# Performance work log

Hardware: AMD Instinct MI355X
Metric: run time of the kernel (lower is better)

Reference implementation:

```python
import jax, jax.numpy as jnp
import numpy as np

B, T, A, I, H = 256, 128, 4, 128, 256


def setup_inputs() -> dict:
    key = jax.random.key(0)
    ks = jax.random.split(key, 6)
    x = jax.random.normal(ks[0], (B, T, A, I), jnp.float32)
    is_init = jax.random.randint(ks[1], (B, T, 1), 0, 2).astype(bool)
    s = 1.0 / np.sqrt(H)  # torch GRUCell init range
    W_ih = jax.random.uniform(ks[2], (3 * H, I), jnp.float32, -s, s)
    W_hh = jax.random.uniform(ks[3], (3 * H, H), jnp.float32, -s, s)
    b_ih = jax.random.uniform(ks[4], (3 * H,), jnp.float32, -s, s)
    b_hh = jax.random.uniform(ks[5], (3 * H,), jnp.float32, -s, s)
    return dict(x=x, is_init=is_init, W_ih=W_ih, W_hh=W_hh, b_ih=b_ih, b_hh=b_hh)


def _gru_forward(x, is_init, W_ih, W_hh, b_ih, b_hh):
    Bb, Tt, Aa, Ii = x.shape
    Hh = W_hh.shape[1]
    # Precompute input projections for all steps: [B,T,A,3H]
    gi = jnp.einsum('btai,ki->btak', x, W_ih) + b_ih
    # is_init [B,T,1] -> per-agent reset mask [B,T,A,1]
    init = jnp.broadcast_to(is_init[:, :, None, :], (Bb, Tt, Aa, 1))
    h0 = jnp.zeros((Bb, Aa, Hh), x.dtype)

    def step(h, inp):
        gi_t, init_t = inp  # [B,A,3H], [B,A,1]
        h = jnp.where(init_t, 0.0, h)  # per-step reset before the cell
        gh = jnp.einsum('bah,kh->bak', h, W_hh) + b_hh
        i_r, i_z, i_n = jnp.split(gi_t, 3, axis=-1)
        h_r, h_z, h_n = jnp.split(gh, 3, axis=-1)
        r = jax.nn.sigmoid(i_r + h_r)
        z = jax.nn.sigmoid(i_z + h_z)
        n = jnp.tanh(i_n + r * h_n)
        h_new = (1.0 - z) * n + z * h
        return h_new, h_new

    _, hs = jax.lax.scan(step, h0, (jnp.moveaxis(gi, 1, 0), jnp.moveaxis(init, 1, 0)))
    return jnp.moveaxis(hs, 0, 1)  # [B,T,A,H]


def reference(x, is_init, W_ih, W_hh, b_ih, b_hh):
    output = _gru_forward(x, is_init, W_ih, W_hh, b_ih, b_hh)
    h_n = output[:, -1]  # [B,A,H]
    return (output, h_n)
```

## Files before the change

kernel.cpp:

```cpp
#include <hip/hip_runtime.h>
#include <cstdint>
#include <cstddef>

#define BB 256
#define TT 128
#define AA 4
#define II 128
#define HH 256
#define K3 768

typedef __attribute__((ext_vector_type(8))) short short8;
typedef __attribute__((ext_vector_type(4))) float f32x4;
typedef __attribute__((ext_vector_type(4))) unsigned short ushort4_t;

#define LGKM_BARRIER() asm volatile("s_waitcnt lgkmcnt(0)\n\ts_barrier" ::: "memory")

static __device__ __forceinline__ unsigned short f2bf(float f) {
  unsigned int b = __float_as_uint(f);
  return (unsigned short)((b + 0x7FFFu + ((b >> 16) & 1u)) >> 16);
}
static __device__ __forceinline__ float bf2f(unsigned short u) {
  return __uint_as_float(((unsigned int)u) << 16);
}

__global__ void wconv_kernel(const float* __restrict__ wih,
                             const float* __restrict__ whh,
                             unsigned short* __restrict__ o) {
  int i = blockIdx.x * 512 + threadIdx.x;
  float v = (i < K3 * II) ? wih[i] : whh[i - K3 * II];
  o[i] = f2bf(v);
}

__global__ __launch_bounds__(512, 2) void gi_kernel(
    const float* __restrict__ x,
    const float* __restrict__ bih_g,
    const float* __restrict__ bhh_g,
    const unsigned short* __restrict__ wb,
    unsigned short* __restrict__ gi) {
  __shared__ alignas(16) unsigned short xs[64][144];
  __shared__ alignas(16) unsigned short gst[16][792];
  __shared__ float bihs[K3];

  const int tid = threadIdx.x;
  const int l = tid & 63, w = tid >> 6;
  const int c = l & 15, g = l >> 4;
  const size_t m0 = (size_t)blockIdx.x * 64;

  for (int i = tid; i < K3; i += 512)
    bihs[i] = bih_g[i] + (i < 2 * HH ? bhh_g[i] : 0.f);
  for (int i = tid; i < 64 * 128; i += 512) {
    int row = i >> 7, col = i & 127;
    xs[row][col] = f2bf(x[m0 * 128 + i]);
  }
  short8 wf[6][4];
#pragma unroll
  for (int kt = 0; kt < 6; ++kt) {
    int row = 96 * w + kt * 16 + c;
#pragma unroll
    for (int kk = 0; kk < 4; ++kk)
      wf[kt][kk] = *(const short8*)&wb[(size_t)row * II + kk * 32 + g * 8];
  }
  LGKM_BARRIER();

  for (int chunk = 0; chunk < 4; ++chunk) {
    short8 bx[4];
#pragma unroll
    for (int kk = 0; kk < 4; ++kk)
      bx[kk] = *(const short8*)&xs[chunk * 16 + c][kk * 32 + g * 8];
    f32x4 acc[6];
#pragma unroll
    for (int kt = 0; kt < 6; ++kt) acc[kt] = (f32x4){0.f, 0.f, 0.f, 0.f};
#pragma unroll
    for (int kt = 0; kt < 6; ++kt)
#pragma unroll
      for (int kk = 0; kk < 4; ++kk)
        acc[kt] = __builtin_amdgcn_mfma_f32_16x16x32_bf16(wf[kt][kk], bx[kk], acc[kt], 0, 0, 0);
#pragma unroll
    for (int kt = 0; kt < 6; ++kt) {
      int gate0 = 96 * w + kt * 16 + g * 4;
      ushort4_t p;
#pragma unroll
      for (int r = 0; r < 4; ++r) p[r] = f2bf(acc[kt][r] + bihs[gate0 + r]);
      *(ushort4_t*)&gst[c][gate0] = p;
    }
    LGKM_BARRIER();
    for (int i = tid; i < 16 * 96; i += 512) {
      int row = i / 96, seg = i - row * 96;
      *(short8*)(gi + (m0 + chunk * 16 + row) * K3 + seg * 8) =
          *(const short8*)&gst[row][seg * 8];
    }
    LGKM_BARRIER();
  }
}

__global__ __launch_bounds__(512, 2) void rnn_kernel(
    const void* __restrict__ init_raw,
    const float* __restrict__ bhh_g,
    const unsigned short* __restrict__ wsb,
    const unsigned short* __restrict__ gi,
    float* __restrict__ out) {
  extern __shared__ char smem[];
  unsigned short* wlN = (unsigned short*)smem;
  unsigned short* hsb = (unsigned short*)(smem + 131072);
  float* scr = (float*)(smem + 135168);
  unsigned char* msk = (unsigned char*)(smem + 147968);
  int* detf = (int*)(smem + 148096);

  const int tid = threadIdx.x;
  const int b = blockIdx.x;
  const unsigned short* whh_b = wsb + K3 * II;

  if (tid < 3) detf[tid] = 0;
  for (int i = tid; i < 2048; i += 512) hsb[i] = 0;
  for (int e = tid; e < 8192; e += 512) {
    int w2 = e >> 10, n = (e >> 9) & 1, kk = (e >> 6) & 7, l2 = e & 63;
    int row = 512 + 32 * w2 + 16 * n + (l2 & 15);
    int col = kk * 32 + (l2 >> 4) * 8;
    *(short8*)(wlN + (size_t)e * 8) = *(const short8*)&whh_b[(size_t)row * HH + col];
  }

  {
    const unsigned int* wq = (const unsigned int*)init_raw;
    int notf = 0, gt1 = 0, oddnz = 0;
    for (int i = tid; i < (BB * TT / 4); i += 512) {
      unsigned int v = wq[i];
      notf |= (v != 0u && v != 0x3F800000u);
      gt1 |= (v > 1u);
      if (i & 1) oddnz |= (v != 0u);
    }
    if (notf) atomicOr(&detf[0], 1);
    if (gt1) atomicOr(&detf[1], 1);
    if (oddnz) atomicOr(&detf[2], 1);
  }
  __syncthreads();
  if (tid < TT) {
    int layout = (!detf[0]) ? 1 : (detf[1] ? 0 : (detf[2] ? 1 : 2));
    int e = b * TT + tid;
    unsigned int v;
    if (layout == 0)      v = ((const unsigned char*)init_raw)[e];
    else if (layout == 1) v = ((const unsigned int*)init_raw)[e];
    else                  v = ((const unsigned int*)init_raw)[2 * e];
    msk[tid] = v ? 1 : 0;
  }

  const int l = tid & 63, w = tid >> 6;
  const int c = l & 15, g = l >> 4;
  const bool act = (c < AA);

  short8 wreg[4][8];
#pragma unroll
  for (int q = 0; q < 4; ++q) {
    int row = (q >> 1) * 256 + 32 * w + (q & 1) * 16 + c;
#pragma unroll
    for (int kk = 0; kk < 8; ++kk)
      wreg[q][kk] = *(const short8*)&whh_b[(size_t)row * HH + kk * 32 + g * 8];
  }

  const int a = g;
  const int u2 = 2 * c;
  const int j0 = 32 * w + u2;
  const float2 bn2 = *(const float2*)&bhh_g[2 * HH + j0];

  __syncthreads();

  const unsigned short* gp = gi + ((size_t)(b * TT) * AA + a) * K3 + j0;
  float* op = out + ((size_t)(b * TT) * AA + a) * HH + j0;
  const unsigned short* hrd = hsb + ((c & 3) * 4 + g) * 8;
  unsigned short* hwp = hsb + w * 128 + a * 32 + u2;
  float* swp = scr + w * 400 + c * 100 + g * 4;
  const float* srp = scr + w * 400 + a * 100 + u2;
  const unsigned short* wlp = wlN + w * 8192 + l * 8;

  float h0 = 0.f, h1 = 0.f;
  unsigned int gcA[3], gcB[3];
  int mA, mB;
  const f32x4 Z4 = {0.f, 0.f, 0.f, 0.f};

#define GI_LOAD(GC)                               \
  do {                                            \
    GC[0] = *(const unsigned int*)(gp);           \
    GC[1] = *(const unsigned int*)(gp + 256);     \
    GC[2] = *(const unsigned int*)(gp + 512);     \
    gp += AA * K3;                                \
  } while (0)

#define L2E 1.44269504088896f

#define STEP(P, GC, MK)                                                           \
  do {                                                                            \
    float sR0, sR1, sZ0, sZ1, sN0, sN1;                                           \
    if ((MK) != 0) {                                                              \
      h0 = 0.f; h1 = 0.f;                                                         \
      sR0 = sR1 = sZ0 = sZ1 = sN0 = sN1 = 0.f;                                    \
    } else {                                                                      \
      short8 bhf[8];                                                              \
      _Pragma("unroll") for (int kk = 0; kk < 8; ++kk)                            \
          bhf[kk] = *(const short8*)(hrd + (P) * 1024 + kk * 128);                \
      f32x4 aR0 = __builtin_amdgcn_mfma_f32_16x16x32_bf16(wreg[0][0], bhf[0], Z4, 0, 0, 0); \
      f32x4 aR1 = __builtin_amdgcn_mfma_f32_16x16x32_bf16(wreg[1][0], bhf[0], Z4, 0, 0, 0); \
      f32x4 aZ0 = __builtin_amdgcn_mfma_f32_16x16x32_bf16(wreg[2][0], bhf[0], Z4, 0, 0, 0); \
      f32x4 aZ1 = __builtin_amdgcn_mfma_f32_16x16x32_bf16(wreg[3][0], bhf[0], Z4, 0, 0, 0); \
      f32x4 aN0 = __builtin_amdgcn_mfma_f32_16x16x32_bf16(                        \
          *(const short8*)(wlp), bhf[0], Z4, 0, 0, 0);                            \
      f32x4 aN1 = __builtin_amdgcn_mfma_f32_16x16x32_bf16(                        \
          *(const short8*)(wlp + 4096), bhf[0], Z4, 0, 0, 0);                     \
      _Pragma("unroll") for (int kk = 1; kk < 8; ++kk) {                          \
        aR0 = __builtin_amdgcn_mfma_f32_16x16x32_bf16(wreg[0][kk], bhf[kk], aR0, 0, 0, 0); \
        aR1 = __builtin_amdgcn_mfma_f32_16x16x32_bf16(wreg[1][kk], bhf[kk], aR1, 0, 0, 0); \
        aZ0 = __builtin_amdgcn_mfma_f32_16x16x32_bf16(wreg[2][kk], bhf[kk], aZ0, 0, 0, 0); \
        aZ1 = __builtin_amdgcn_mfma_f32_16x16x32_bf16(wreg[3][kk], bhf[kk], aZ1, 0, 0, 0); \
        aN0 = __builtin_amdgcn_mfma_f32_16x16x32_bf16(                            \
            *(const short8*)(wlp + kk * 512), bhf[kk], aN0, 0, 0, 0);             \
        aN1 = __builtin_amdgcn_mfma_f32_16x16x32_bf16(                            \
            *(const short8*)(wlp + 4096 + kk * 512), bhf[kk], aN1, 0, 0, 0);      \
      }                                                                           \
      if (act) {                                                                  \
        *(f32x4*)(swp + 0)  = aR0;                                                \
        *(f32x4*)(swp + 16) = aR1;                                                \
        *(f32x4*)(swp + 32) = aZ0;                                                \
        *(f32x4*)(swp + 48) = aZ1;                                                \
        *(f32x4*)(swp + 64) = aN0;                                                \
        *(f32x4*)(swp + 80) = aN1;                                                \
      }                                                                           \
      float2 vR = *(const float2*)(srp);                                          \
      float2 vZ = *(const float2*)(srp + 32);                                     \
      float2 vN = *(const float2*)(srp + 64);                                     \
      sR0 = vR.x; sR1 = vR.y; sZ0 = vZ.x; sZ1 = vZ.y; sN0 = vN.x; sN1 = vN.y;     \
    }                                                                             \
    const float gr0 = bf2f((unsigned short)(GC[0]));                              \
    const float gr1 = bf2f((unsigned short)(GC[0] >> 16));                        \
    const float gz0 = bf2f((unsigned short)(GC[1]));                              \
    const float gz1 = bf2f((unsigned short)(GC[1] >> 16));                        \
    const float gn0 = bf2f((unsigned short)(GC[2]));                              \
    const float gn1 = bf2f((unsigned short)(GC[2] >> 16));                        \
    const float rs0 = __builtin_amdgcn_rcpf(1.f + __builtin_amdgcn_exp2f(-(gr0 + sR0) * L2E)); \
    const float rs1 = __builtin_amdgcn_rcpf(1.f + __builtin_amdgcn_exp2f(-(gr1 + sR1) * L2E)); \
    const float zs0 = __builtin_amdgcn_rcpf(1.f + __builtin_amdgcn_exp2f(-(gz0 + sZ0) * L2E)); \
    const float zs1 = __builtin_amdgcn_rcpf(1.f + __builtin_amdgcn_exp2f(-(gz1 + sZ1) * L2E)); \
    const float pre0 = gn0 + rs0 * (sN0 + bn2.x);                                 \
    const float pre1 = gn1 + rs1 * (sN1 + bn2.y);                                 \
    const float nn0 = 1.f - 2.f * __builtin_amdgcn_rcpf(1.f + __builtin_amdgcn_exp2f(pre0 * (2.f * L2E))); \
    const float nn1 = 1.f - 2.f * __builtin_amdgcn_rcpf(1.f + __builtin_amdgcn_exp2f(pre1 * (2.f * L2E))); \
    h0 = fmaf(zs0, h0 - nn0, nn0);                                                \
    h1 = fmaf(zs1, h1 - nn1, nn1);                                                \
    unsigned int hw = (unsigned int)f2bf(h0) | ((unsigned int)f2bf(h1) << 16);    \
    *(unsigned int*)(hwp + (1 - (P)) * 1024) = hw;                                \
    float2 o2; o2.x = h0; o2.y = h1;                                              \
    *(float2*)op = o2;                                                            \
    op += AA * HH;                                                                \
    LGKM_BARRIER();                                                               \
  } while (0)

  GI_LOAD(gcA);
  mA = msk[0];
  for (int t = 0; t < TT - 2; t += 2) {
    GI_LOAD(gcB);
    mB = msk[t + 1];
    STEP(0, gcA, mA);
    GI_LOAD(gcA);
    mA = msk[t + 2];
    STEP(1, gcB, mB);
  }
  {
    GI_LOAD(gcB);
    mB = msk[TT - 1];
    STEP(0, gcA, mA);
    STEP(1, gcB, mB);
  }

  {
    float* hp = out + (size_t)BB * TT * AA * HH + ((size_t)b * AA + a) * HH + j0;
    float2 o2; o2.x = h0; o2.y = h1;
    *(float2*)hp = o2;
  }
#undef GI_LOAD
#undef STEP
}

template <int WSW>
__global__ __launch_bounds__(512, 2) void gru_kernel(
    const float* __restrict__ x,
    const void* __restrict__ init_raw,
    const float* __restrict__ wih_f,
    const float* __restrict__ whh_f,
    const float* __restrict__ bih_g,
    const float* __restrict__ bhh_g,
    const unsigned short* __restrict__ wb,
    float* __restrict__ out) {
  __shared__ alignas(16) unsigned short xs[AA][II + 8];
  __shared__ alignas(16) unsigned short hsb[AA][HH + 8];
  __shared__ float hs32[AA][HH];
  __shared__ float gi_s[K3][5];
  __shared__ float gh_s[K3][5];
  __shared__ float bihs[K3];
  __shared__ float bhhs[K3];
  __shared__ unsigned char msk[TT];
  __shared__ int detf[3];

  const int tid = threadIdx.x;
  const int b = blockIdx.x;

  if (tid < 3) detf[tid] = 0;
  for (int i = tid; i < K3; i += 512) { bihs[i] = bih_g[i]; bhhs[i] = bhh_g[i]; }
  for (int i = tid; i < AA * HH; i += 512) {
    hs32[i >> 8][i & 255] = 0.f;
    hsb[i >> 8][i & 255] = 0;
  }
  __syncthreads();
  {
    const unsigned int* wq = (const unsigned int*)init_raw;
    int notf = 0, gt1 = 0, oddnz = 0;
    for (int i = tid; i < (BB * TT / 4); i += 512) {
      unsigned int v = wq[i];
      notf |= (v != 0u && v != 0x3F800000u);
      gt1 |= (v > 1u);
      if (i & 1) oddnz |= (v != 0u);
    }
    if (notf) atomicOr(&detf[0], 1);
    if (gt1) atomicOr(&detf[1], 1);
    if (oddnz) atomicOr(&detf[2], 1);
  }
  __syncthreads();
  if (tid < TT) {
    int layout = (!detf[0]) ? 1 : (detf[1] ? 0 : (detf[2] ? 1 : 2));
    int e = b * TT + tid;
    unsigned int v;
    if (layout == 0)      v = ((const unsigned char*)init_raw)[e];
    else if (layout == 1) v = ((const unsigned int*)init_raw)[e];
    else                  v = ((const unsigned int*)init_raw)[2 * e];
    msk[tid] = v ? 1 : 0;
  }
  __syncthreads();

  const int l = tid & 63;
  const int w = tid >> 6;
  const int c = l & 15;
  const int g = l >> 4;
  const bool act = (c < AA);
  const int xa = tid >> 7, xi = tid & 127;
  const float* xrow = x + (size_t)b * TT * AA * II;
  const unsigned short* wihb = wb;
  const unsigned short* whhb = wb + K3 * II;

  for (int t = 0; t < TT; ++t) {
    xs[xa][xi] = f2bf(xrow[(size_t)t * (AA * II) + tid]);
    if (msk[t]) {
      for (int i = tid; i < AA * HH; i += 512) {
        hs32[i >> 8][i & 255] = 0.f;
        hsb[i >> 8][i & 255] = 0;
      }
    }
    __syncthreads();

    short8 bx[4], bh[8];
    if (act) {
#pragma unroll
      for (int kk = 0; kk < 4; ++kk) bx[kk] = *(const short8*)&xs[c][kk * 32 + g * 8];
#pragma unroll
      for (int kk = 0; kk < 8; ++kk) bh[kk] = *(const short8*)&hsb[c][kk * 32 + g * 8];
    } else {
#pragma unroll
      for (int kk = 0; kk < 4; ++kk) bx[kk] = (short8)0;
#pragma unroll
      for (int kk = 0; kk < 8; ++kk) bh[kk] = (short8)0;
    }

#pragma unroll
    for (int kt = 0; kt < 6; ++kt) {
      const int ar = w * 96 + kt * 16 + c;
      f32x4 acc = {0.f, 0.f, 0.f, 0.f};
#pragma unroll
      for (int kk = 0; kk < 4; ++kk) {
        short8 aw;
        if (WSW) {
          aw = *(const short8*)&wihb[(size_t)ar * II + kk * 32 + g * 8];
        } else {
          const float* p = &wih_f[(size_t)ar * II + kk * 32 + g * 8];
#pragma unroll
          for (int e = 0; e < 8; ++e) aw[e] = (short)f2bf(p[e]);
        }
        acc = __builtin_amdgcn_mfma_f32_16x16x32_bf16(aw, bx[kk], acc, 0, 0, 0);
      }
      if (act) {
        const int dr = w * 96 + kt * 16 + g * 4;
#pragma unroll
        for (int r = 0; r < 4; ++r) gi_s[dr + r][c] = acc[r];
      }
    }

#pragma unroll
    for (int kt = 0; kt < 6; ++kt) {
      const int ar = w * 96 + kt * 16 + c;
      f32x4 acc = {0.f, 0.f, 0.f, 0.f};
#pragma unroll
      for (int kk = 0; kk < 8; ++kk) {
        short8 aw;
        if (WSW) {
          aw = *(const short8*)&whhb[(size_t)ar * HH + kk * 32 + g * 8];
        } else {
          const float* p = &whh_f[(size_t)ar * HH + kk * 32 + g * 8];
#pragma unroll
          for (int e = 0; e < 8; ++e) aw[e] = (short)f2bf(p[e]);
        }
        acc = __builtin_amdgcn_mfma_f32_16x16x32_bf16(aw, bh[kk], acc, 0, 0, 0);
      }
      if (act) {
        const int dr = w * 96 + kt * 16 + g * 4;
#pragma unroll
        for (int r = 0; r < 4; ++r) gh_s[dr + r][c] = acc[r];
      }
    }
    __syncthreads();

#pragma unroll
    for (int it = 0; it < 2; ++it) {
      const int idx = it * 512 + tid;
      const int a = idx >> 8, j = idx & 255;
      const float ir = gi_s[j][a] + bihs[j];
      const float iz = gi_s[HH + j][a] + bihs[HH + j];
      const float inn = gi_s[2 * HH + j][a] + bihs[2 * HH + j];
      const float hr = gh_s[j][a] + bhhs[j];
      const float hz = gh_s[HH + j][a] + bhhs[HH + j];
      const float hn = gh_s[2 * HH + j][a] + bhhs[2 * HH + j];
      const float r = 1.f / (1.f + __expf(-(ir + hr)));
      const float z = 1.f / (1.f + __expf(-(iz + hz)));
      const float pre = inn + r * hn;
      const float ea = __expf(-2.f * fabsf(pre));
      float n = (1.f - ea) / (1.f + ea);
      n = (pre < 0.f) ? -n : n;
      const float hold = hs32[a][j];
      const float hnew = (1.f - z) * n + z * hold;
      hs32[a][j] = hnew;
      hsb[a][j] = f2bf(hnew);
      out[(((size_t)b * TT + t) * AA + a) * HH + j] = hnew;
      if (t == TT - 1)
        out[(size_t)BB * TT * AA * HH + ((size_t)b * AA + a) * HH + j] = hnew;
    }
    __syncthreads();
  }
}

extern "C" void kernel_launch(void* const* d_in, const int* in_sizes, int n_in,
                              void* d_out, int out_size, void* d_ws, size_t ws_size,
                              hipStream_t stream) {
  (void)in_sizes; (void)n_in; (void)out_size;
  const float* x = (const float*)d_in[0];
  const void* is_init = d_in[1];
  const float* wih = (const float*)d_in[2];
  const float* whh = (const float*)d_in[3];
  const float* bih = (const float*)d_in[4];
  const float* bhh = (const float*)d_in[5];
  float* out = (float*)d_out;

  const size_t W_ELS = (size_t)(K3 * II + K3 * HH);
  const size_t W_BYTES = W_ELS * 2;
  const size_t GI_BYTES = (size_t)BB * TT * AA * K3 * 2;
  const int SMEM = 148112;

  if (ws_size >= W_BYTES + GI_BYTES) {
    hipError_t e = hipFuncSetAttribute(
        (const void*)rnn_kernel, hipFuncAttributeMaxDynamicSharedMemorySize, SMEM);
    if (e == hipSuccess) {
      unsigned short* wb = (unsigned short*)d_ws;
      unsigned short* gi = wb + W_ELS;
      wconv_kernel<<<(int)(W_ELS / 512), 512, 0, stream>>>(wih, whh, wb);
      gi_kernel<<<2048, 512, 0, stream>>>(x, bih, bhh, wb, gi);
      rnn_kernel<<<BB, 512, SMEM, stream>>>(is_init, bhh, wb, gi, out);
      return;
    }
  }
  if (ws_size >= W_BYTES) {
    unsigned short* wb = (unsigned short*)d_ws;
    wconv_kernel<<<(int)(W_ELS / 512), 512, 0, stream>>>(wih, whh, wb);
    gru_kernel<1><<<BB, 512, 0, stream>>>(x, is_init, wih, whh, bih, bhh, wb, out);
  } else {
    gru_kernel<0><<<BB, 512, 0, stream>>>(x, is_init, wih, whh, bih, bhh, nullptr, out);
  }
}
```

Baseline: 243.8 us.

## Split each sequence into independent segments at reset points and run them concurrently

Every reset in the mask sets the hidden state to zero, so the sequence is cut at the first reset after positions 32, 64 and 96 into up to four independent segments. These segments fill the 12 MFMA columns that were previously padding (only 4 of 16 were used). The recurrence then runs for only the longest segment length instead of all 128 steps. It also removes the scratch round-trip through shared memory by computing gates straight from the MFMA accumulators, and loads the input projections per step. The gain depends on how reset positions fall in the data, and the per-lane bookkeeping adds branches.

Result: no change. 246.6 us (+1.2%).

```diff
diff --git a/kernel.cpp b/kernel.cpp
--- a/kernel.cpp
+++ b/kernel.cpp
@@ -102,21 +102,21 @@
   extern __shared__ char smem[];
   unsigned short* wlN = (unsigned short*)smem;
   unsigned short* hsb = (unsigned short*)(smem + 131072);
-  float* scr = (float*)(smem + 135168);
-  unsigned char* msk = (unsigned char*)(smem + 147968);
-  int* detf = (int*)(smem + 148096);
+  unsigned char* mskL = (unsigned char*)(smem + 147456);
+  int* bnd = (int*)(smem + 147592);
+  int* detf = (int*)(smem + 147612);
 
   const int tid = threadIdx.x;
   const int b = blockIdx.x;
   const unsigned short* whh_b = wsb + K3 * II;
 
   if (tid < 3) detf[tid] = 0;
-  for (int i = tid; i < 2048; i += 512) hsb[i] = 0;
-  for (int e = tid; e < 8192; e += 512) {
-    int w2 = e >> 10, n = (e >> 9) & 1, kk = (e >> 6) & 7, l2 = e & 63;
+  for (int i = tid; i < 8192; i += 512) hsb[i] = 0;
+  for (int f = tid; f < 8192; f += 512) {
+    int w2 = f >> 10, n = (f >> 9) & 1, kk = (f >> 6) & 7, l2 = f & 63;
     int row = 512 + 32 * w2 + 16 * n + (l2 & 15);
     int col = kk * 32 + (l2 >> 4) * 8;
-    *(short8*)(wlN + (size_t)e * 8) = *(const short8*)&whh_b[(size_t)row * HH + col];
+    *(short8*)(wlN + (size_t)f * 8) = *(const short8*)&whh_b[(size_t)row * HH + col];
   }
 
   {
@@ -140,12 +140,21 @@
     if (layout == 0)      v = ((const unsigned char*)init_raw)[e];
     else if (layout == 1) v = ((const unsigned int*)init_raw)[e];
     else                  v = ((const unsigned int*)init_raw)[2 * e];
-    msk[tid] = v ? 1 : 0;
-  }
+    mskL[tid] = v ? 1 : 0;
+  }
+  if (tid == TT) mskL[TT] = 1;
+  __syncthreads();
+  if (tid < 3) {
+    int target = 32 * (tid + 1);
+    int bb = TT;
+    for (int t = target; t < TT; ++t)
+      if (mskL[t]) { bb = t; break; }
+    bnd[tid + 1] = bb;
+  }
+  if (tid == 3) { bnd[0] = 0; bnd[4] = TT; }
 
   const int l = tid & 63, w = tid >> 6;
   const int c = l & 15, g = l >> 4;
-  const bool act = (c < AA);
 
   short8 wreg[4][8];
 #pragma unroll
@@ -155,125 +164,108 @@
     for (int kk = 0; kk < 8; ++kk)
       wreg[q][kk] = *(const short8*)&whh_b[(size_t)row * HH + kk * 32 + g * 8];
   }
-
-  const int a = g;
-  const int u2 = 2 * c;
-  const int j0 = 32 * w + u2;
-  const float2 bn2 = *(const float2*)&bhh_g[2 * HH + j0];
-
-  __syncthreads();
-
-  const unsigned short* gp = gi + ((size_t)(b * TT) * AA + a) * K3 + j0;
-  float* op = out + ((size_t)(b * TT) * AA + a) * HH + j0;
-  const unsigned short* hrd = hsb + ((c & 3) * 4 + g) * 8;
-  unsigned short* hwp = hsb + w * 128 + a * 32 + u2;
-  float* swp = scr + w * 400 + c * 100 + g * 4;
-  const float* srp = scr + w * 400 + a * 100 + u2;
+  __syncthreads();
+
+  const int a = c & 3, q = c >> 2;
+  const int j0 = 32 * w + g * 4;
+  int tcur = bnd[q];
+  int trem = bnd[q + 1] - tcur;
+  int maxlen = bnd[1] - bnd[0];
+  { int l1 = bnd[2] - bnd[1]; if (l1 > maxlen) maxlen = l1;
+    int l2 = bnd[3] - bnd[2]; if (l2 > maxlen) maxlen = l2;
+    int l3 = TT - bnd[3];     if (l3 > maxlen) maxlen = l3; }
+  const int taddr = (tcur < TT) ? tcur : (TT - 1);
+  const unsigned short* gp = gi + ((size_t)(b * TT + taddr) * AA + a) * K3 + j0;
+  float* op = out + ((size_t)(b * TT + taddr) * AA + a) * HH + j0;
+  f32x4 bn[2];
+  bn[0] = *(const f32x4*)&bhh_g[2 * HH + j0];
+  bn[1] = *(const f32x4*)&bhh_g[2 * HH + j0 + 16];
+  float* hnp = out + (size_t)BB * TT * AA * HH + ((size_t)b * AA + a) * HH + j0;
+
+  const unsigned short* hrd = hsb + c * 32 + g * 8;
+  unsigned short* hw1 = hsb + w * 512 + c * 32 + (g >> 1) * 8 + (g & 1) * 4;
   const unsigned short* wlp = wlN + w * 8192 + l * 8;
 
-  float h0 = 0.f, h1 = 0.f;
-  unsigned int gcA[3], gcB[3];
-  int mA, mB;
+  f32x4 hold[2];
+  hold[0] = (f32x4){0.f, 0.f, 0.f, 0.f};
+  hold[1] = (f32x4){0.f, 0.f, 0.f, 0.f};
   const f32x4 Z4 = {0.f, 0.f, 0.f, 0.f};
 
-#define GI_LOAD(GC)                               \
-  do {                                            \
-    GC[0] = *(const unsigned int*)(gp);           \
-    GC[1] = *(const unsigned int*)(gp + 256);     \
-    GC[2] = *(const unsigned int*)(gp + 512);     \
-    gp += AA * K3;                                \
-  } while (0)
-
 #define L2E 1.44269504088896f
 
-#define STEP(P, GC, MK)                                                           \
+#define STEP(P)                                                                   \
   do {                                                                            \
-    float sR0, sR1, sZ0, sZ1, sN0, sN1;                                           \
-    if ((MK) != 0) {                                                              \
-      h0 = 0.f; h1 = 0.f;                                                         \
-      sR0 = sR1 = sZ0 = sZ1 = sN0 = sN1 = 0.f;                                    \
-    } else {                                                                      \
-      short8 bhf[8];                                                              \
-      _Pragma("unroll") for (int kk = 0; kk < 8; ++kk)                            \
-          bhf[kk] = *(const short8*)(hrd + (P) * 1024 + kk * 128);                \
-      f32x4 aR0 = __builtin_amdgcn_mfma_f32_16x16x32_bf16(wreg[0][0], bhf[0], Z4, 0, 0, 0); \
-      f32x4 aR1 = __builtin_amdgcn_mfma_f32_16x16x32_bf16(wreg[1][0], bhf[0], Z4, 0, 0, 0); \
-      f32x4 aZ0 = __builtin_amdgcn_mfma_f32_16x16x32_bf16(wreg[2][0], bhf[0], Z4, 0, 0, 0); \
-      f32x4 aZ1 = __builtin_amdgcn_mfma_f32_16x16x32_bf16(wreg[3][0], bhf[0], Z4, 0, 0, 0); \
-      f32x4 aN0 = __builtin_amdgcn_mfma_f32_16x16x32_bf16(                        \
-          *(const short8*)(wlp), bhf[0], Z4, 0, 0, 0);                            \
-      f32x4 aN1 = __builtin_amdgcn_mfma_f32_16x16x32_bf16(                        \
-          *(const short8*)(wlp + 4096), bhf[0], Z4, 0, 0, 0);                     \
-      _Pragma("unroll") for (int kk = 1; kk < 8; ++kk) {                          \
-        aR0 = __builtin_amdgcn_mfma_f32_16x16x32_bf16(wreg[0][kk], bhf[kk], aR0, 0, 0, 0); \
-        aR1 = __builtin_amdgcn_mfma_f32_16x16x32_bf16(wreg[1][kk], bhf[kk], aR1, 0, 0, 0); \
-        aZ0 = __builtin_amdgcn_mfma_f32_16x16x32_bf16(wreg[2][kk], bhf[kk], aZ0, 0, 0, 0); \
-        aZ1 = __builtin_amdgcn_mfma_f32_16x16x32_bf16(wreg[3][kk], bhf[kk], aZ1, 0, 0, 0); \
-        aN0 = __builtin_amdgcn_mfma_f32_16x16x32_bf16(                            \
-            *(const short8*)(wlp + kk * 512), bhf[kk], aN0, 0, 0, 0);             \
-        aN1 = __builtin_amdgcn_mfma_f32_16x16x32_bf16(                            \
-            *(const short8*)(wlp + 4096 + kk * 512), bhf[kk], aN1, 0, 0, 0);      \
-      }                                                                           \
-      if (act) {                                                                  \
-        *(f32x4*)(swp + 0)  = aR0;                                                \
-        *(f32x4*)(swp + 16) = aR1;                                                \
-        *(f32x4*)(swp + 32) = aZ0;                                                \
-        *(f32x4*)(swp + 48) = aZ1;                                                \
-        *(f32x4*)(swp + 64) = aN0;                                                \
-        *(f32x4*)(swp + 80) = aN1;                                                \
-      }                                                                           \
-      float2 vR = *(const float2*)(srp);                                          \
-      float2 vZ = *(const float2*)(srp + 32);                                     \
-      float2 vN = *(const float2*)(srp + 64);                                     \
-      sR0 = vR.x; sR1 = vR.y; sZ0 = vZ.x; sZ1 = vZ.y; sN0 = vN.x; sN1 = vN.y;     \
+    ushort4_t gr0 = *(const ushort4_t*)(gp);                                      \
+    ushort4_t gr1 = *(const ushort4_t*)(gp + 16);                                 \
+    ushort4_t gz0 = *(const ushort4_t*)(gp + 256);                                \
+    ushort4_t gz1 = *(const ushort4_t*)(gp + 272);                                \
+    ushort4_t gn0 = *(const ushort4_t*)(gp + 512);                                \
+    ushort4_t gn1 = *(const ushort4_t*)(gp + 528);                                \
+    short8 bhf[8];                                                                \
+    _Pragma("unroll") for (int kk = 0; kk < 8; ++kk)                              \
+        bhf[kk] = *(const short8*)(hrd + (P) * 4096 + kk * 512);                  \
+    f32x4 aR0 = __builtin_amdgcn_mfma_f32_16x16x32_bf16(wreg[0][0], bhf[0], Z4, 0, 0, 0); \
+    f32x4 aR1 = __builtin_amdgcn_mfma_f32_16x16x32_bf16(wreg[1][0], bhf[0], Z4, 0, 0, 0); \
+    f32x4 aZ0 = __builtin_amdgcn_mfma_f32_16x16x32_bf16(wreg[2][0], bhf[0], Z4, 0, 0, 0); \
+    f32x4 aZ1 = __builtin_amdgcn_mfma_f32_16x16x32_bf16(wreg[3][0], bhf[0], Z4, 0, 0, 0); \
+    f32x4 aN0 = __builtin_amdgcn_mfma_f32_16x16x32_bf16(*(const short8*)(wlp), bhf[0], Z4, 0, 0, 0); \
+    f32x4 aN1 = __builtin_amdgcn_mfma_f32_16x16x32_bf16(*(const short8*)(wlp + 4096), bhf[0], Z4, 0, 0, 0); \
+    _Pragma("unroll") for (int kk = 1; kk < 8; ++kk) {                            \
+      aR0 = __builtin_amdgcn_mfma_f32_16x16x32_bf16(wreg[0][kk], bhf[kk], aR0, 0, 0, 0); \
+      aR1 = __builtin_amdgcn_mfma_f32_16x16x32_bf16(wreg[1][kk], bhf[kk], aR1, 0, 0, 0); \
+      aZ0 = __builtin_amdgcn_mfma_f32_16x16x32_bf16(wreg[2][kk], bhf[kk], aZ0, 0, 0, 0); \
+      aZ1 = __builtin_amdgcn_mfma_f32_16x16x32_bf16(wreg[3][kk], bhf[kk], aZ1, 0, 0, 0); \
+      aN0 = __builtin_amdgcn_mfma_f32_16x16x32_bf16(*(const short8*)(wlp + kk * 512), bhf[kk], aN0, 0, 0, 0); \
+      aN1 = __builtin_amdgcn_mfma_f32_16x16x32_bf16(*(const short8*)(wlp + 4096 + kk * 512), bhf[kk], aN1, 0, 0, 0); \
     }                                                                             \
-    const float gr0 = bf2f((unsigned short)(GC[0]));                              \
-    const float gr1 = bf2f((unsigned short)(GC[0] >> 16));                        \
-    const float gz0 = bf2f((unsigned short)(GC[1]));                              \
-    const float gz1 = bf2f((unsigned short)(GC[1] >> 16));                        \
-    const float gn0 = bf2f((unsigned short)(GC[2]));                              \
-    const float gn1 = bf2f((unsigned short)(GC[2] >> 16));                        \
-    const float rs0 = __builtin_amdgcn_rcpf(1.f + __builtin_amdgcn_exp2f(-(gr0 + sR0) * L2E)); \
-    const float rs1 = __builtin_amdgcn_rcpf(1.f + __builtin_amdgcn_exp2f(-(gr1 + sR1) * L2E)); \
-    const float zs0 = __builtin_amdgcn_rcpf(1.f + __builtin_amdgcn_exp2f(-(gz0 + sZ0) * L2E)); \
-    const float zs1 = __builtin_amdgcn_rcpf(1.f + __builtin_amdgcn_exp2f(-(gz1 + sZ1) * L2E)); \
-    const float pre0 = gn0 + rs0 * (sN0 + bn2.x);                                 \
-    const float pre1 = gn1 + rs1 * (sN1 + bn2.y);                                 \
-    const float nn0 = 1.f - 2.f * __builtin_amdgcn_rcpf(1.f + __builtin_amdgcn_exp2f(pre0 * (2.f * L2E))); \
-    const float nn1 = 1.f - 2.f * __builtin_amdgcn_rcpf(1.f + __builtin_amdgcn_exp2f(pre1 * (2.f * L2E))); \
-    h0 = fmaf(zs0, h0 - nn0, nn0);                                                \
-    h1 = fmaf(zs1, h1 - nn1, nn1);                                                \
-    unsigned int hw = (unsigned int)f2bf(h0) | ((unsigned int)f2bf(h1) << 16);    \
-    *(unsigned int*)(hwp + (1 - (P)) * 1024) = hw;                                \
-    float2 o2; o2.x = h0; o2.y = h1;                                              \
-    *(float2*)op = o2;                                                            \
-    op += AA * HH;                                                                \
+    f32x4 hnv0, hnv1;                                                             \
+    ushort4_t hb0, hb1;                                                           \
+    _Pragma("unroll") for (int r = 0; r < 4; ++r) {                               \
+      const float pr = bf2f(gr0[r]) + aR0[r];                                     \
+      const float pz = bf2f(gz0[r]) + aZ0[r];                                     \
+      const float rs = __builtin_amdgcn_rcpf(1.f + __builtin_amdgcn_exp2f(-pr * L2E)); \
+      const float zs = __builtin_amdgcn_rcpf(1.f + __builtin_amdgcn_exp2f(-pz * L2E)); \
+      const float hn = aN0[r] + bn[0][r];                                         \
+      const float pre = bf2f(gn0[r]) + rs * hn;                                   \
+      const float nn = 1.f - 2.f * __builtin_amdgcn_rcpf(1.f + __builtin_amdgcn_exp2f(pre * (2.f * L2E))); \
+      const float hv = fmaf(zs, hold[0][r] - nn, nn);                             \
+      hnv0[r] = hv; hb0[r] = f2bf(hv);                                            \
+    }                                                                             \
+    _Pragma("unroll") for (int r = 0; r < 4; ++r) {                               \
+      const float pr = bf2f(gr1[r]) + aR1[r];                                     \
+      const float pz = bf2f(gz1[r]) + aZ1[r];                                     \
+      const float rs = __builtin_amdgcn_rcpf(1.f + __builtin_amdgcn_exp2f(-pr * L2E)); \
+      const float zs = __builtin_amdgcn_rcpf(1.f + __builtin_amdgcn_exp2f(-pz * L2E)); \
+      const float hn = aN1[r] + bn[1][r];                                         \
+      const float pre = bf2f(gn1[r]) + rs * hn;                                   \
+      const float nn = 1.f - 2.f * __builtin_amdgcn_rcpf(1.f + __builtin_amdgcn_exp2f(pre * (2.f * L2E))); \
+      const float hv = fmaf(zs, hold[1][r] - nn, nn);                             \
+      hnv1[r] = hv; hb1[r] = f2bf(hv);                                            \
+    }                                                                             \
+    hold[0] = hnv0; hold[1] = hnv1;                                               \
+    const bool active = (trem > 0);                                               \
+    if (active) {                                                                 \
+      *(f32x4*)op = hnv0;                                                         \
+      *(f32x4*)(op + 16) = hnv1;                                                  \
+      if (tcur == TT - 1) { *(f32x4*)hnp = hnv0; *(f32x4*)(hnp + 16) = hnv1; }    \
+      tcur += 1; trem -= 1;                                                       \
+      if (trem > 0) { gp += AA * K3; op += AA * HH; }                             \
+    }                                                                             \
+    const int mn = mskL[tcur];                                                    \
+    if (mn) {                                                                     \
+      hb0 = (ushort4_t)0; hb1 = (ushort4_t)0;                                     \
+      hold[0] = Z4; hold[1] = Z4;                                                 \
+    }                                                                             \
+    *(ushort4_t*)(hw1 + (1 - (P)) * 4096) = hb0;                                  \
+    *(ushort4_t*)(hw1 + 16 + (1 - (P)) * 4096) = hb1;                             \
     LGKM_BARRIER();                                                               \
   } while (0)
 
-  GI_LOAD(gcA);
-  mA = msk[0];
-  for (int t = 0; t < TT - 2; t += 2) {
-    GI_LOAD(gcB);
-    mB = msk[t + 1];
-    STEP(0, gcA, mA);
-    GI_LOAD(gcA);
-    mA = msk[t + 2];
-    STEP(1, gcB, mB);
-  }
-  {
-    GI_LOAD(gcB);
-    mB = msk[TT - 1];
-    STEP(0, gcA, mA);
-    STEP(1, gcB, mB);
-  }
-
-  {
-    float* hp = out + (size_t)BB * TT * AA * HH + ((size_t)b * AA + a) * HH + j0;
-    float2 o2; o2.x = h0; o2.y = h1;
-    *(float2*)hp = o2;
-  }
-#undef GI_LOAD
+  const int nsteps = (maxlen + 1) & ~1;
+  for (int i = 0; i < nsteps; i += 2) {
+    STEP(0);
+    STEP(1);
+  }
 #undef STEP
 }
 
@@ -455,7 +447,7 @@
   const size_t W_ELS = (size_t)(K3 * II + K3 * HH);
   const size_t W_BYTES = W_ELS * 2;
   const size_t GI_BYTES = (size_t)BB * TT * AA * K3 * 2;
-  const int SMEM = 148112;
+  const int SMEM = 147632;
 
   if (ws_size >= W_BYTES + GI_BYTES) {
     hipError_t e = hipFuncSetAttribute(
```
